# Performance work log

Hardware: AMD Instinct MI355X
Metric: run time of the kernel (lower is better)

Reference implementation:

```python
import jax, jax.numpy as jnp
import numpy as np

C0 = 32        # num_feat_maps[0]
LD = 6         # latent_dim
NC = 1         # num_classes
B, P = 1, 96


def setup_inputs() -> dict:
    key = jax.random.key(0)
    ks = jax.random.split(key, 10)
    s = lambda fan_in: 1.0 / np.sqrt(fan_in)
    return {
        "feature_map": jax.random.normal(ks[0], (B, C0, P, P, P), dtype=jnp.float32),
        "z": jax.random.normal(ks[1], (B, LD), dtype=jnp.float32),
        "w1": jax.random.normal(ks[2], (C0, C0 + LD), dtype=jnp.float32) * s(C0 + LD),
        "b1": jnp.zeros((C0,), dtype=jnp.float32),
        "w2": jax.random.normal(ks[3], (C0, C0), dtype=jnp.float32) * s(C0),
        "b2": jnp.zeros((C0,), dtype=jnp.float32),
        "w3": jax.random.normal(ks[4], (C0, C0), dtype=jnp.float32) * s(C0),
        "b3": jnp.zeros((C0,), dtype=jnp.float32),
        "wl": jax.random.normal(ks[5], (NC, C0), dtype=jnp.float32) * s(C0),
        "bl": jnp.zeros((NC,), dtype=jnp.float32),
    }


def _pw(x, w, b):
    # 1x1x1 conv3d == pointwise channel GEMM: [B,Ci,X,Y,Z] x [Co,Ci] -> [B,Co,X,Y,Z]
    return jnp.einsum('bcxyz,oc->boxyz', x, w) + b[None, :, None, None, None]


def reference(feature_map, z, w1, b1, w2, b2, w3, b3, wl, bl):
    b, _, x_, y_, z_ = feature_map.shape
    # tile() on the unsqueezed z is equivalent to broadcasting over spatial dims
    zb = jnp.broadcast_to(z[:, :, None, None, None], (b, z.shape[1], x_, y_, z_))
    h = jnp.concatenate([feature_map, zb], axis=1)          # [B, C0+LD, P,P,P]
    h = jax.nn.relu(_pw(h, w1, b1))
    h = jax.nn.relu(_pw(h, w2, b2))
    h = jax.nn.relu(_pw(h, w3, b3))
    return _pw(h, wl, bl)                                    # [B, NC, P,P,P]
```

## Files before the change

### kernel.cpp

```cpp
#include <hip/hip_runtime.h>


typedef float    f32x16 __attribute__((ext_vector_type(16)));
typedef short    bf16x8 __attribute__((ext_vector_type(8)));
typedef unsigned u32x4  __attribute__((ext_vector_type(4)));

constexpr int NPTS  = 96 * 96 * 96;
constexpr int BLOCK = 256;
constexpr int NBLK  = NPTS / (32 * (BLOCK / 64));

__device__ __forceinline__ unsigned cvtpk(float lo, float hi) {
    unsigned d;
    asm("v_cvt_pk_bf16_f32 %0, %1, %2" : "=v"(d) : "v"(lo), "v"(hi));
    return d;
}
__device__ __forceinline__ float unlo(unsigned d) { return __uint_as_float(d << 16); }

__device__ __forceinline__ bf16x8 mk4(unsigned a, unsigned b, unsigned c, unsigned d) {
    u32x4 u; u.x = a; u.y = b; u.z = c; u.w = d;
    return __builtin_bit_cast(bf16x8, u);
}

__device__ __forceinline__ void swap32(unsigned a, unsigned b, unsigned& x, unsigned& y) {
    auto r = __builtin_amdgcn_permlane32_swap(a, b, false, false);
    x = r[0]; y = r[1];
}

__device__ __forceinline__ void load_wsplit(const float* __restrict__ W, int stride,
                                            int row, int koff, bf16x8& Hf, bf16x8& Lf) {
    const float2* p2 = reinterpret_cast<const float2*>(W + row * stride + koff);
    float2 q0 = p2[0], q1 = p2[1], q2 = p2[2], q3 = p2[3];
    unsigned h0 = cvtpk(q0.x, q0.y), h1 = cvtpk(q1.x, q1.y);
    unsigned h2 = cvtpk(q2.x, q2.y), h3 = cvtpk(q3.x, q3.y);
    unsigned l0 = cvtpk(q0.x - unlo(h0), q0.y - __uint_as_float(h0 & 0xffff0000u));
    unsigned l1 = cvtpk(q1.x - unlo(h1), q1.y - __uint_as_float(h1 & 0xffff0000u));
    unsigned l2 = cvtpk(q2.x - unlo(h2), q2.y - __uint_as_float(h2 & 0xffff0000u));
    unsigned l3 = cvtpk(q3.x - unlo(h3), q3.y - __uint_as_float(h3 & 0xffff0000u));
    Hf = mk4(h0, h1, h2, h3);
    Lf = mk4(l0, l1, l2, l3);
}

__device__ __forceinline__ void pack_frags(const f32x16 acc, bf16x8& F0, bf16x8& F1) {
    unsigned p0 = cvtpk(fmaxf(acc[0],  0.f), fmaxf(acc[1],  0.f));
    unsigned p1 = cvtpk(fmaxf(acc[2],  0.f), fmaxf(acc[3],  0.f));
    unsigned p2 = cvtpk(fmaxf(acc[4],  0.f), fmaxf(acc[5],  0.f));
    unsigned p3 = cvtpk(fmaxf(acc[6],  0.f), fmaxf(acc[7],  0.f));
    unsigned p4 = cvtpk(fmaxf(acc[8],  0.f), fmaxf(acc[9],  0.f));
    unsigned p5 = cvtpk(fmaxf(acc[10], 0.f), fmaxf(acc[11], 0.f));
    unsigned p6 = cvtpk(fmaxf(acc[12], 0.f), fmaxf(acc[13], 0.f));
    unsigned p7 = cvtpk(fmaxf(acc[14], 0.f), fmaxf(acc[15], 0.f));
    unsigned a0, a1, b0, b1, c0, c1, d0, d1;
    swap32(p0, p2, a0, a1); swap32(p1, p3, b0, b1);
    swap32(p4, p6, c0, c1); swap32(p5, p7, d0, d1);
    F0 = mk4(a0, b0, a1, b1);
    F1 = mk4(c0, d0, c1, d1);
}

__device__ __forceinline__ unsigned bias_word(float b) {
    float bhi = unlo(cvtpk(b, b));
    return cvtpk(b, b - bhi);
}

#define WLAYER(acc, WH0, WL0, WH1, WL1, F0, F1)                                   \
    acc = __builtin_amdgcn_mfma_f32_32x32x16_bf16(WH0, F0, acc, 0, 0, 0);         \
    acc = __builtin_amdgcn_mfma_f32_32x32x16_bf16(WL0, F0, acc, 0, 0, 0);         \
    acc = __builtin_amdgcn_mfma_f32_32x32x16_bf16(WH1, F1, acc, 0, 0, 0);         \
    acc = __builtin_amdgcn_mfma_f32_32x32x16_bf16(WL1, F1, acc, 0, 0, 0);

__global__ __launch_bounds__(BLOCK, 3)
void fused_mlp_mfma(const float* __restrict__ fm, const float* __restrict__ z,
                    const float* __restrict__ w1, const float* __restrict__ b1,
                    const float* __restrict__ w2, const float* __restrict__ b2,
                    const float* __restrict__ w3, const float* __restrict__ b3,
                    const float* __restrict__ wl, const float* __restrict__ bl,
                    float* __restrict__ out)
{
    const int lane = threadIdx.x & 63;
    const int wid  = blockIdx.x * (BLOCK / 64) + (threadIdx.x >> 6);
    const int hl   = lane >> 5;
    const int col  = lane & 31;
    const int koff = 8 * hl;
    const int pt   = wid * 32 + col;

    float v[16];
    #pragma unroll
    for (int i = 0; i < 8; ++i) v[i]     = fm[(koff + i) * NPTS + pt];
    #pragma unroll
    for (int i = 0; i < 8; ++i) v[8 + i] = fm[(16 + koff + i) * NPTS + pt];

    bf16x8 W1h0, W1l0, W1h1, W1l1, W2h0, W2l0, W2h1, W2l1, W3h0, W3l0, W3h1, W3l1;
    load_wsplit(w1, 38, col, 0  + koff, W1h0, W1l0);
    load_wsplit(w1, 38, col, 16 + koff, W1h1, W1l1);
    load_wsplit(w2, 32, col, 0  + koff, W2h0, W2l0);
    load_wsplit(w2, 32, col, 16 + koff, W2h1, W2l1);
    load_wsplit(w3, 32, col, 0  + koff, W3h0, W3l0);
    load_wsplit(w3, 32, col, 16 + koff, W3h1, W3l1);

    float b1e = b1[col];
    b1e = fmaf(w1[col * 38 + 32], z[0], b1e);
    b1e = fmaf(w1[col * 38 + 33], z[1], b1e);
    b1e = fmaf(w1[col * 38 + 34], z[2], b1e);
    b1e = fmaf(w1[col * 38 + 35], z[3], b1e);
    b1e = fmaf(w1[col * 38 + 36], z[4], b1e);
    b1e = fmaf(w1[col * 38 + 37], z[5], b1e);
    const unsigned zero = 0u;
    bf16x8 Ab1  = mk4(hl ? zero : bias_word(b1e),     zero, zero, zero);
    bf16x8 Ab2  = mk4(hl ? zero : bias_word(b2[col]), zero, zero, zero);
    bf16x8 Ab3  = mk4(hl ? zero : bias_word(b3[col]), zero, zero, zero);
    bf16x8 Bone = mk4(hl ? zero : 0x3F803F80u,        zero, zero, zero);

    f32x16 wlr;
    #pragma unroll
    for (int r = 0; r < 16; ++r) wlr[r] = wl[(r & 3) + 8 * (r >> 2) + 4 * hl];
    const float blv = bl[0];

    f32x16 zacc;
    #pragma unroll
    for (int r = 0; r < 16; ++r) zacc[r] = 0.f;

    bf16x8 F0 = mk4(cvtpk(v[0],  v[1]),  cvtpk(v[2],  v[3]),
                    cvtpk(v[4],  v[5]),  cvtpk(v[6],  v[7]));
    bf16x8 F1 = mk4(cvtpk(v[8],  v[9]),  cvtpk(v[10], v[11]),
                    cvtpk(v[12], v[13]), cvtpk(v[14], v[15]));
    f32x16 acc = __builtin_amdgcn_mfma_f32_32x32x16_bf16(Ab1, Bone, zacc, 0, 0, 0);
    WLAYER(acc, W1h0, W1l0, W1h1, W1l1, F0, F1)

    pack_frags(acc, F0, F1);
    acc = __builtin_amdgcn_mfma_f32_32x32x16_bf16(Ab2, Bone, zacc, 0, 0, 0);
    WLAYER(acc, W2h0, W2l0, W2h1, W2l1, F0, F1)

    pack_frags(acc, F0, F1);
    acc = __builtin_amdgcn_mfma_f32_32x32x16_bf16(Ab3, Bone, zacc, 0, 0, 0);
    WLAYER(acc, W3h0, W3l0, W3h1, W3l1, F0, F1)

    float s = 0.f;
    #pragma unroll
    for (int r = 0; r < 16; ++r) s = fmaf(wlr[r], fmaxf(acc[r], 0.f), s);
    unsigned px, py;
    swap32(__float_as_uint(s), __float_as_uint(s), px, py);
    float tot = __uint_as_float(px) + __uint_as_float(py) + blv;
    if (lane < 32) out[pt] = tot;
}

extern "C" void kernel_launch(void* const* d_in, const int* in_sizes, int n_in,
                              void* d_out, int out_size, void* d_ws, size_t ws_size,
                              hipStream_t stream)
{
    const float* fm = (const float*)d_in[0];
    const float* z  = (const float*)d_in[1];
    const float* w1 = (const float*)d_in[2];
    const float* b1 = (const float*)d_in[3];
    const float* w2 = (const float*)d_in[4];
    const float* b2 = (const float*)d_in[5];
    const float* w3 = (const float*)d_in[6];
    const float* b3 = (const float*)d_in[7];
    const float* wl = (const float*)d_in[8];
    const float* bl = (const float*)d_in[9];
    float* out = (float*)d_out;

    fused_mlp_mfma<<<NBLK, BLOCK, 0, stream>>>(
        fm, z, w1, b1, w2, b2, w3, b3, wl, bl, out);
}
```

Measured before the change: 192.2 us.

## Stage feature-map tile in LDS via async global_load_lds, process four groups per wave

Each block now loads a 512-point by 32-channel tile of the feature map straight into shared memory with 16-byte direct global-to-LDS loads. Each wave then runs four 32-point groups, reading its inputs from LDS. This replaces the narrow per-lane 4-byte global loads with wide coalesced ones and spreads the weight-split setup over more points per wave. In exchange it uses 64KB of LDS per block, lowers launch-bounds occupancy from 3 to 2, and adds a block-wide barrier with no overlap between loading and compute.

New measurement: 187.5 us. -2.4%, faster.

```diff
diff --git a/kernel.cpp b/kernel.cpp
--- a/kernel.cpp
+++ b/kernel.cpp
@@ -6,8 +6,12 @@
 typedef unsigned u32x4  __attribute__((ext_vector_type(4)));
 
 constexpr int NPTS  = 96 * 96 * 96;
+constexpr int TILE  = 512;
 constexpr int BLOCK = 256;
-constexpr int NBLK  = NPTS / (32 * (BLOCK / 64));
+constexpr int NBLK  = NPTS / TILE;
+
+typedef __attribute__((address_space(1))) const void glob_void;
+typedef __attribute__((address_space(3))) void lds_void;
 
 __device__ __forceinline__ unsigned cvtpk(float lo, float hi) {
     unsigned d;
@@ -67,7 +71,7 @@
     acc = __builtin_amdgcn_mfma_f32_32x32x16_bf16(WH1, F1, acc, 0, 0, 0);         \
     acc = __builtin_amdgcn_mfma_f32_32x32x16_bf16(WL1, F1, acc, 0, 0, 0);
 
-__global__ __launch_bounds__(BLOCK, 3)
+__global__ __launch_bounds__(BLOCK, 2)
 void fused_mlp_mfma(const float* __restrict__ fm, const float* __restrict__ z,
                     const float* __restrict__ w1, const float* __restrict__ b1,
                     const float* __restrict__ w2, const float* __restrict__ b2,
@@ -75,18 +79,25 @@
                     const float* __restrict__ wl, const float* __restrict__ bl,
                     float* __restrict__ out)
 {
+    __shared__ float lds[32][TILE];
+
     const int lane = threadIdx.x & 63;
-    const int wid  = blockIdx.x * (BLOCK / 64) + (threadIdx.x >> 6);
+    const int w    = threadIdx.x >> 6;
     const int hl   = lane >> 5;
     const int col  = lane & 31;
     const int koff = 8 * hl;
-    const int pt   = wid * 32 + col;
+    const int tb   = blockIdx.x * TILE;
 
-    float v[16];
     #pragma unroll
-    for (int i = 0; i < 8; ++i) v[i]     = fm[(koff + i) * NPTS + pt];
-    #pragma unroll
-    for (int i = 0; i < 8; ++i) v[8 + i] = fm[(16 + koff + i) * NPTS + pt];
+    for (int i = 0; i < 16; ++i) {
+        const int idx = w * 16 + i;
+        const int c   = idx >> 1;
+        const int h   = idx & 1;
+        const float* gsrc = fm + c * NPTS + tb + h * 256 + lane * 4;
+        __builtin_amdgcn_global_load_lds((glob_void*)gsrc,
+                                         (lds_void*)&lds[c][h * 256],
+                                         16, 0, 0);
+    }
 
     bf16x8 W1h0, W1l0, W1h1, W1l1, W2h0, W2l0, W2h1, W2l1, W3h0, W3l0, W3h1, W3l1;
     load_wsplit(w1, 38, col, 0  + koff, W1h0, W1l0);
@@ -118,28 +129,45 @@
     #pragma unroll
     for (int r = 0; r < 16; ++r) zacc[r] = 0.f;
 
-    bf16x8 F0 = mk4(cvtpk(v[0],  v[1]),  cvtpk(v[2],  v[3]),
-                    cvtpk(v[4],  v[5]),  cvtpk(v[6],  v[7]));
-    bf16x8 F1 = mk4(cvtpk(v[8],  v[9]),  cvtpk(v[10], v[11]),
-                    cvtpk(v[12], v[13]), cvtpk(v[14], v[15]));
-    f32x16 acc = __builtin_amdgcn_mfma_f32_32x32x16_bf16(Ab1, Bone, zacc, 0, 0, 0);
-    WLAYER(acc, W1h0, W1l0, W1h1, W1l1, F0, F1)
+    __syncthreads();
 
-    pack_frags(acc, F0, F1);
-    acc = __builtin_amdgcn_mfma_f32_32x32x16_bf16(Ab2, Bone, zacc, 0, 0, 0);
-    WLAYER(acc, W2h0, W2l0, W2h1, W2l1, F0, F1)
+    #pragma unroll
+    for (int g = 0; g < 4; ++g) {
+        const int pl = (w * 4 + g) * 32 + col;
 
-    pack_frags(acc, F0, F1);
-    acc = __builtin_amdgcn_mfma_f32_32x32x16_bf16(Ab3, Bone, zacc, 0, 0, 0);
-    WLAYER(acc, W3h0, W3l0, W3h1, W3l1, F0, F1)
+        float v0  = lds[koff + 0][pl],  v1  = lds[koff + 1][pl];
+        float v2  = lds[koff + 2][pl],  v3  = lds[koff + 3][pl];
+        float v4  = lds[koff + 4][pl],  v5  = lds[koff + 5][pl];
+        float v6  = lds[koff + 6][pl],  v7  = lds[koff + 7][pl];
+        float v8  = lds[16 + koff + 0][pl], v9  = lds[16 + koff + 1][pl];
+        float v10 = lds[16 + koff + 2][pl], v11 = lds[16 + koff + 3][pl];
+        float v12 = lds[16 + koff + 4][pl], v13 = lds[16 + koff + 5][pl];
+        float v14 = lds[16 + koff + 6][pl], v15 = lds[16 + koff + 7][pl];
 
-    float s = 0.f;
-    #pragma unroll
-    for (int r = 0; r < 16; ++r) s = fmaf(wlr[r], fmaxf(acc[r], 0.f), s);
-    unsigned px, py;
-    swap32(__float_as_uint(s), __float_as_uint(s), px, py);
-    float tot = __uint_as_float(px) + __uint_as_float(py) + blv;
-    if (lane < 32) out[pt] = tot;
+        bf16x8 F0 = mk4(cvtpk(v0, v1),  cvtpk(v2, v3),
+                        cvtpk(v4, v5),  cvtpk(v6, v7));
+        bf16x8 F1 = mk4(cvtpk(v8, v9),  cvtpk(v10, v11),
+                        cvtpk(v12, v13), cvtpk(v14, v15));
+
+        f32x16 acc = __builtin_amdgcn_mfma_f32_32x32x16_bf16(Ab1, Bone, zacc, 0, 0, 0);
+        WLAYER(acc, W1h0, W1l0, W1h1, W1l1, F0, F1)
+
+        pack_frags(acc, F0, F1);
+        acc = __builtin_amdgcn_mfma_f32_32x32x16_bf16(Ab2, Bone, zacc, 0, 0, 0);
+        WLAYER(acc, W2h0, W2l0, W2h1, W2l1, F0, F1)
+
+        pack_frags(acc, F0, F1);
+        acc = __builtin_amdgcn_mfma_f32_32x32x16_bf16(Ab3, Bone, zacc, 0, 0, 0);
+        WLAYER(acc, W3h0, W3l0, W3h1, W3l1, F0, F1)
+
+        float s = 0.f;
+        #pragma unroll
+        for (int r = 0; r < 16; ++r) s = fmaf(wlr[r], fmaxf(acc[r], 0.f), s);
+        unsigned px, py;
+        swap32(__float_as_uint(s), __float_as_uint(s), px, py);
+        float tot = __uint_as_float(px) + __uint_as_float(py) + blv;
+        if (lane < 32) out[tb + pl] = tot;
+    }
 }
 
 extern "C" void kernel_launch(void* const* d_in, const int* in_sizes, int n_in,
```

## Process four point groups per wave with software-pipelined feature-map loads

Applied to the files above, without the earlier changes.

Each wave now handles four 32-point groups instead of one, so the per-wave weight splitting, bias setup and wl loads are paid once across four groups. Loads for the next groups are issued before the MFMA chain of the current group runs, overlapping global-memory latency with compute. In exchange the grid is four times smaller and each wave holds more live registers, which could lower occupancy under the launch bound of 3.

New measurement: 185.2 us. 1.04x faster.

```diff
diff --git a/kernel.cpp b/kernel.cpp
--- a/kernel.cpp
+++ b/kernel.cpp
@@ -7,7 +7,8 @@
 
 constexpr int NPTS  = 96 * 96 * 96;
 constexpr int BLOCK = 256;
-constexpr int NBLK  = NPTS / (32 * (BLOCK / 64));
+constexpr int GPW   = 4;
+constexpr int NBLK  = NPTS / (32 * GPW * (BLOCK / 64));
 
 __device__ __forceinline__ unsigned cvtpk(float lo, float hi) {
     unsigned d;
@@ -67,6 +68,36 @@
     acc = __builtin_amdgcn_mfma_f32_32x32x16_bf16(WH1, F1, acc, 0, 0, 0);         \
     acc = __builtin_amdgcn_mfma_f32_32x32x16_bf16(WL1, F1, acc, 0, 0, 0);
 
+#define LOADG(arr, pt)                                                            \
+    _Pragma("unroll")                                                             \
+    for (int i = 0; i < 8; ++i) {                                                 \
+        arr[i]     = fm[(koff + i) * NPTS + (pt)];                                \
+        arr[8 + i] = fm[(16 + koff + i) * NPTS + (pt)];                           \
+    }
+
+#define COMPUTE(arr, pt)                                                          \
+    {                                                                             \
+        bf16x8 F0 = mk4(cvtpk(arr[0],  arr[1]),  cvtpk(arr[2],  arr[3]),          \
+                        cvtpk(arr[4],  arr[5]),  cvtpk(arr[6],  arr[7]));         \
+        bf16x8 F1 = mk4(cvtpk(arr[8],  arr[9]),  cvtpk(arr[10], arr[11]),         \
+                        cvtpk(arr[12], arr[13]), cvtpk(arr[14], arr[15]));        \
+        f32x16 acc = __builtin_amdgcn_mfma_f32_32x32x16_bf16(Ab1, Bone, zacc, 0, 0, 0); \
+        WLAYER(acc, W1h0, W1l0, W1h1, W1l1, F0, F1)                               \
+        pack_frags(acc, F0, F1);                                                  \
+        acc = __builtin_amdgcn_mfma_f32_32x32x16_bf16(Ab2, Bone, zacc, 0, 0, 0);  \
+        WLAYER(acc, W2h0, W2l0, W2h1, W2l1, F0, F1)                               \
+        pack_frags(acc, F0, F1);                                                  \
+        acc = __builtin_amdgcn_mfma_f32_32x32x16_bf16(Ab3, Bone, zacc, 0, 0, 0);  \
+        WLAYER(acc, W3h0, W3l0, W3h1, W3l1, F0, F1)                               \
+        float s = 0.f;                                                            \
+        _Pragma("unroll")                                                         \
+        for (int r = 0; r < 16; ++r) s = fmaf(wlr[r], fmaxf(acc[r], 0.f), s);     \
+        unsigned px, py;                                                          \
+        swap32(__float_as_uint(s), __float_as_uint(s), px, py);                   \
+        float tot = __uint_as_float(px) + __uint_as_float(py) + blv;              \
+        if (lane < 32) out[pt] = tot;                                             \
+    }
+
 __global__ __launch_bounds__(BLOCK, 3)
 void fused_mlp_mfma(const float* __restrict__ fm, const float* __restrict__ z,
                     const float* __restrict__ w1, const float* __restrict__ b1,
@@ -80,13 +111,15 @@
     const int hl   = lane >> 5;
     const int col  = lane & 31;
     const int koff = 8 * hl;
-    const int pt   = wid * 32 + col;
 
-    float v[16];
-    #pragma unroll
-    for (int i = 0; i < 8; ++i) v[i]     = fm[(koff + i) * NPTS + pt];
-    #pragma unroll
-    for (int i = 0; i < 8; ++i) v[8 + i] = fm[(16 + koff + i) * NPTS + pt];
+    const int p0 = (wid * GPW + 0) * 32 + col;
+    const int p1 = (wid * GPW + 1) * 32 + col;
+    const int p2 = (wid * GPW + 2) * 32 + col;
+    const int p3 = (wid * GPW + 3) * 32 + col;
+
+    float va[16], vb[16];
+    LOADG(va, p0)
+    LOADG(vb, p1)
 
     bf16x8 W1h0, W1l0, W1h1, W1l1, W2h0, W2l0, W2h1, W2l1, W3h0, W3l0, W3h1, W3l1;
     load_wsplit(w1, 38, col, 0  + koff, W1h0, W1l0);
@@ -118,28 +151,16 @@
     #pragma unroll
     for (int r = 0; r < 16; ++r) zacc[r] = 0.f;
 
-    bf16x8 F0 = mk4(cvtpk(v[0],  v[1]),  cvtpk(v[2],  v[3]),
-                    cvtpk(v[4],  v[5]),  cvtpk(v[6],  v[7]));
-    bf16x8 F1 = mk4(cvtpk(v[8],  v[9]),  cvtpk(v[10], v[11]),
-                    cvtpk(v[12], v[13]), cvtpk(v[14], v[15]));
-    f32x16 acc = __builtin_amdgcn_mfma_f32_32x32x16_bf16(Ab1, Bone, zacc, 0, 0, 0);
-    WLAYER(acc, W1h0, W1l0, W1h1, W1l1, F0, F1)
+    float vc[16];
+    LOADG(vc, p2)
+    COMPUTE(va, p0)
 
-    pack_frags(acc, F0, F1);
-    acc = __builtin_amdgcn_mfma_f32_32x32x16_bf16(Ab2, Bone, zacc, 0, 0, 0);
-    WLAYER(acc, W2h0, W2l0, W2h1, W2l1, F0, F1)
+    float vd[16];
+    LOADG(vd, p3)
+    COMPUTE(vb, p1)
 
-    pack_frags(acc, F0, F1);
-    acc = __builtin_amdgcn_mfma_f32_32x32x16_bf16(Ab3, Bone, zacc, 0, 0, 0);
-    WLAYER(acc, W3h0, W3l0, W3h1, W3l1, F0, F1)
-
-    float s = 0.f;
-    #pragma unroll
-    for (int r = 0; r < 16; ++r) s = fmaf(wlr[r], fmaxf(acc[r], 0.f), s);
-    unsigned px, py;
-    swap32(__float_as_uint(s), __float_as_uint(s), px, py);
-    float tot = __uint_as_float(px) + __uint_as_float(py) + blv;
-    if (lane < 32) out[pt] = tot;
+    COMPUTE(vc, p2)
+    COMPUTE(vd, p3)
 }
 
 extern "C" void kernel_launch(void* const* d_in, const int* in_sizes, int n_in,
```
